# Kernel optimization log

Measured on AMD Instinct MI355X. Metric: run time of the kernel, lower is better.

Reference implementation:

```python
import jax, jax.numpy as jnp
import numpy as np
from jax import lax

N_KERNELS = 10000
KS = 9
DILATIONS = (1, 2, 4, 8, 16)   # static dilation groups, 2000 kernels each
GROUP = N_KERNELS // len(DILATIONS)
BN_EPS = 1e-5


def setup_inputs() -> dict:
    key = jax.random.key(0)
    kx, kw, kb, klw = jax.random.split(key, 4)
    B, L, C, n_class = 16, 256, 3, 10
    x_enc = jax.random.normal(kx, (B, L, C), dtype=jnp.float32)
    # ROCKET kernels: normal weights, mean-centered per kernel
    W = jax.random.normal(kw, (N_KERNELS, C, KS), dtype=jnp.float32)
    W = W - W.mean(axis=(1, 2), keepdims=True)
    # ROCKET biases: uniform(-1, 1)
    b = jax.random.uniform(kb, (N_KERNELS,), dtype=jnp.float32) * 2.0 - 1.0
    gamma = jnp.ones((2 * N_KERNELS,), dtype=jnp.float32)
    beta = jnp.zeros((2 * N_KERNELS,), dtype=jnp.float32)
    linW = jax.random.normal(klw, (2 * N_KERNELS, n_class), dtype=jnp.float32) * 0.01
    linB = jnp.zeros((n_class,), dtype=jnp.float32)
    return {"x_enc": x_enc, "W": W, "b": b, "gamma": gamma, "beta": beta,
            "linW": linW, "linB": linB}


def _rocket_features(x, W, b):
    # x: [B, C, L]; W: [N_KERNELS, C, KS]; b: [N_KERNELS]
    feats = []
    dn = ("NCH", "OIH", "NCH")
    for i, d in enumerate(DILATIONS):
        w = W[i * GROUP:(i + 1) * GROUP]                       # [G, C, KS]
        bb = b[i * GROUP:(i + 1) * GROUP]                      # [G]
        y = lax.conv_general_dilated(x, w, window_strides=(1,),
                                     padding="SAME", rhs_dilation=(d,),
                                     dimension_numbers=dn)      # [B, G, L]
        y = y + bb[None, :, None]
        feats.append(y.max(axis=-1))                            # max pooling
        feats.append(jnp.where(y > 0, 1.0, 0.0).mean(axis=-1))  # PPV
    return jnp.concatenate(feats, axis=-1)                      # [B, 2*N_KERNELS]


def reference(x_enc, W, b, gamma, beta, linW, linB):
    x = jnp.transpose(x_enc, (0, 2, 1))        # [B, C, L]
    feat = _rocket_features(x, W, b)           # [B, 20000]
    # BatchNorm1d (training mode: batch statistics, biased variance)
    mu = feat.mean(axis=0)
    var = feat.var(axis=0)
    feat_n = (feat - mu) * lax.rsqrt(var + BN_EPS) * gamma + beta
    return feat_n @ linW + linB                # [B, num_class]
```

## Files before the change

kernel.cpp:

```cpp
#include <hip/hip_runtime.h>
#include <cmath>

#define NK       10000
#define GROUP    2000
#define SEQ_L    256
#define FEAT_DIM 20000
#define NBATCH   16

typedef _Float16 half8 __attribute__((ext_vector_type(8)));
typedef float    f32x4 __attribute__((ext_vector_type(4)));

__launch_bounds__(128)
__global__ void rocket_mfma(const float* __restrict__ x_enc,
                            const float* __restrict__ Wk,
                            const float* __restrict__ bias,
                            float* __restrict__ feat)
{
    __shared__ __align__(16) float     xp[3 * 384];
    __shared__ __align__(16) _Float16  Bh[4 * 256 * 8];
    __shared__ __align__(16) _Float16  Bl[4 * 256 * 8];

    const int mt  = blockIdx.x;
    const int gi  = blockIdx.y;
    const int b   = blockIdx.z;
    const int d   = 1 << gi;
    const int tid = threadIdx.x;
    const int l   = tid & 63;
    const int wv  = tid >> 6;
    const int kb  = l >> 4;
    const int lr  = l & 15;

    for (int i = tid; i < 3 * 384; i += 128) xp[i] = 0.f;
    __syncthreads();
    for (int e = tid; e < SEQ_L * 3; e += 128) {
        const int t = e / 3;
        const int c = e - t * 3;
        xp[c * 384 + 64 + t] = x_enc[(b * SEQ_L + t) * 3 + c];
    }

    float awf[4][8];
#pragma unroll
    for (int tt = 0; tt < 4; ++tt) {
        const int nl = mt * 128 + wv * 64 + tt * 16 + lr;
        const int n  = gi * GROUP + (nl < GROUP ? nl : GROUP - 1);
#pragma unroll
        for (int j = 0; j < 8; ++j) {
            const int k = kb * 8 + j;
            awf[tt][j] = (k < 27) ? Wk[n * 27 + k] : 0.f;
        }
    }
    half8 ahi[4], alo[4];
#pragma unroll
    for (int tt = 0; tt < 4; ++tt)
#pragma unroll
        for (int j = 0; j < 8; ++j) {
            const _Float16 h = (_Float16)awf[tt][j];
            ahi[tt][j] = h;
            alo[tt][j] = (_Float16)(awf[tt][j] - (float)h);
        }
    float bsv[4][4];
#pragma unroll
    for (int tt = 0; tt < 4; ++tt)
#pragma unroll
        for (int r = 0; r < 4; ++r) {
            const int nl = mt * 128 + wv * 64 + tt * 16 + kb * 4 + r;
            bsv[tt][r] = bias[gi * GROUP + (nl < GROUP ? nl : GROUP - 1)];
        }

    __syncthreads();

    {
        const int kg = tid >> 5;
        const int tl = tid & 31;
#pragma unroll
        for (int i = 0; i < 8; ++i) {
            const int t = tl + 32 * i;
            half8 hv, lv;
#pragma unroll
            for (int kk = 0; kk < 8; ++kk) {
                const int k2 = kg * 8 + kk;
                float v = 0.f;
                if (k2 < 27) {
                    const int c  = (k2 >= 18) ? 2 : (k2 >= 9 ? 1 : 0);
                    const int k9 = k2 - c * 9;
                    v = xp[c * 384 + 64 + t + (k9 - 4) * d];
                }
                const _Float16 h = (_Float16)v;
                hv[kk] = h;
                lv[kk] = (_Float16)(v - (float)h);
            }
            *(half8*)&Bh[(kg * 256 + t) * 8] = hv;
            *(half8*)&Bl[(kg * 256 + t) * 8] = lv;
        }
    }
    __syncthreads();

    float mx[4][4], cnt[4][4];
#pragma unroll
    for (int tt = 0; tt < 4; ++tt)
#pragma unroll
        for (int r = 0; r < 4; ++r) { mx[tt][r] = -INFINITY; cnt[tt][r] = 0.f; }

#pragma unroll
    for (int ch = 0; ch < 16; ++ch) {
        const int t = ch * 16 + lr;
        const half8 bh = *(const half8*)&Bh[(kb * 256 + t) * 8];
        const half8 bl = *(const half8*)&Bl[(kb * 256 + t) * 8];
#pragma unroll
        for (int tt = 0; tt < 4; ++tt) {
            f32x4 acc = {0.f, 0.f, 0.f, 0.f};
            acc = __builtin_amdgcn_mfma_f32_16x16x32_f16(ahi[tt], bh, acc, 0, 0, 0);
            acc = __builtin_amdgcn_mfma_f32_16x16x32_f16(alo[tt], bh, acc, 0, 0, 0);
            acc = __builtin_amdgcn_mfma_f32_16x16x32_f16(ahi[tt], bl, acc, 0, 0, 0);
#pragma unroll
            for (int r = 0; r < 4; ++r) {
                const float y = acc[r] + bsv[tt][r];
                mx[tt][r]  = fmaxf(mx[tt][r], y);
                cnt[tt][r] += (y > 0.f) ? 1.f : 0.f;
            }
        }
    }

#pragma unroll
    for (int tt = 0; tt < 4; ++tt)
#pragma unroll
        for (int r = 0; r < 4; ++r) {
#pragma unroll
            for (int m = 1; m < 16; m <<= 1) {
                mx[tt][r]  = fmaxf(mx[tt][r], __shfl_xor(mx[tt][r], m));
                cnt[tt][r] += __shfl_xor(cnt[tt][r], m);
            }
        }

    if (lr == 0) {
        float* fb = feat + b * FEAT_DIM + gi * 4000;
#pragma unroll
        for (int tt = 0; tt < 4; ++tt)
#pragma unroll
            for (int r = 0; r < 4; ++r) {
                const int nl = mt * 128 + wv * 64 + tt * 16 + kb * 4 + r;
                if (nl < GROUP) {
                    fb[nl]         = mx[tt][r];
                    fb[2000 + nl]  = cnt[tt][r] * (1.0f / 256.0f);
                }
            }
    }
}

__launch_bounds__(256)
__global__ void bn_gemv(const float* __restrict__ feat,
                        const float* __restrict__ gamma,
                        const float* __restrict__ beta,
                        const float* __restrict__ linW,
                        float* __restrict__ partial)
{
    __shared__ float gs[625], hs[625];
    const int sl  = blockIdx.x;
    const int f0  = sl * 625;
    const int tid = threadIdx.x;

    for (int i = tid; i < 625; i += 256) {
        const int f = f0 + i;
        float s = 0.f, ss = 0.f;
#pragma unroll
        for (int b = 0; b < NBATCH; ++b) {
            const float v = feat[b * FEAT_DIM + f];
            s += v; ss += v * v;
        }
        const float mu  = s * (1.f / NBATCH);
        const float var = ss * (1.f / NBATCH) - mu * mu;
        const float gg  = gamma[f] * rsqrtf(var + 1e-5f);
        gs[i] = gg;
        hs[i] = beta[f] - mu * gg;
    }
    __syncthreads();

    const int bb = tid >> 4;
    const int ft = tid & 15;
    float acc[10];
#pragma unroll
    for (int c = 0; c < 10; ++c) acc[c] = 0.f;

    for (int i = ft; i < 625; i += 16) {
        const int f = f0 + i;
        const float tv = fmaf(feat[bb * FEAT_DIM + f], gs[i], hs[i]);
#pragma unroll
        for (int c = 0; c < 10; ++c) acc[c] = fmaf(tv, linW[f * 10 + c], acc[c]);
    }
#pragma unroll
    for (int c = 0; c < 10; ++c)
#pragma unroll
        for (int m = 1; m < 16; m <<= 1) acc[c] += __shfl_xor(acc[c], m);

    if (ft == 0) {
#pragma unroll
        for (int c = 0; c < 10; ++c)
            partial[(sl * NBATCH + bb) * 10 + c] = acc[c];
    }
}

__launch_bounds__(160)
__global__ void gemv_final(const float* __restrict__ partial,
                           const float* __restrict__ linB,
                           float* __restrict__ out)
{
    const int tid = threadIdx.x;
    const int c   = tid % 10;
    float s = linB[c];
#pragma unroll
    for (int sl = 0; sl < 32; ++sl) s += partial[sl * 160 + tid];
    out[tid] = s;
}

extern "C" void kernel_launch(void* const* d_in, const int* in_sizes, int n_in,
                              void* d_out, int out_size, void* d_ws, size_t ws_size,
                              hipStream_t stream) {
    const float* x     = (const float*)d_in[0];
    const float* Wk    = (const float*)d_in[1];
    const float* bias  = (const float*)d_in[2];
    const float* gamma = (const float*)d_in[3];
    const float* beta  = (const float*)d_in[4];
    const float* linW  = (const float*)d_in[5];
    const float* linB  = (const float*)d_in[6];
    float* out = (float*)d_out;

    float* feat    = (float*)d_ws;
    float* partial = feat + NBATCH * FEAT_DIM;

    rocket_mfma<<<dim3(16, 5, NBATCH), 128, 0, stream>>>(x, Wk, bias, feat);
    bn_gemv<<<dim3(32), 256, 0, stream>>>(feat, gamma, beta, linW, partial);
    gemv_final<<<dim3(1), 160, 0, stream>>>(partial, linB, out);
}
```

Baseline: 42.93 us.

## Precompute im2col fp16 split B tiles once per batch/dilation; widen BN-GEMV grid

Moves construction of the dilated im2col B operand (hi/lo fp16 split) out of the MFMA kernel into a separate build_B kernel. That kernel writes the operand once per (dilation, batch) to workspace, so the 16 M-tile blocks no longer each rebuild it in LDS and can read it straight from global/L2. The BN+GEMV stage is split into 80 slices of 250 features instead of 32 slices of 625, giving more parallelism. The cost is an extra kernel launch plus global memory traffic for the B operand.

Result: faster. 36.28 us (-15.5%).

```diff
diff --git a/kernel.cpp b/kernel.cpp
--- a/kernel.cpp
+++ b/kernel.cpp
@@ -10,35 +10,68 @@
 typedef _Float16 half8 __attribute__((ext_vector_type(8)));
 typedef float    f32x4 __attribute__((ext_vector_type(4)));
 
+__launch_bounds__(256)
+__global__ void build_B(const float* __restrict__ x_enc,
+                        _Float16* __restrict__ Bh_g,
+                        _Float16* __restrict__ Bl_g)
+{
+    __shared__ __align__(16) float xp[3 * 384];
+    const int gi  = blockIdx.x;
+    const int b   = blockIdx.y;
+    const int d   = 1 << gi;
+    const int tid = threadIdx.x;
+
+    for (int i = tid; i < 3 * 384; i += 256) xp[i] = 0.f;
+    __syncthreads();
+    for (int e = tid; e < SEQ_L * 3; e += 256) {
+        const int t = e / 3;
+        const int c = e - t * 3;
+        xp[c * 384 + 64 + t] = x_enc[(b * SEQ_L + t) * 3 + c];
+    }
+    __syncthreads();
+
+    const int base = (gi * NBATCH + b) * 1024;
+#pragma unroll
+    for (int q = 0; q < 4; ++q) {
+        const int idx = q * 256 + tid;
+        const int kb  = idx >> 8;
+        const int t   = idx & 255;
+        half8 hv, lv;
+#pragma unroll
+        for (int kk = 0; kk < 8; ++kk) {
+            const int k2 = kb * 8 + kk;
+            float v = 0.f;
+            if (k2 < 27) {
+                const int c  = (k2 >= 18) ? 2 : (k2 >= 9 ? 1 : 0);
+                const int k9 = k2 - c * 9;
+                v = xp[c * 384 + 64 + t + (k9 - 4) * d];
+            }
+            const _Float16 h = (_Float16)v;
+            hv[kk] = h;
+            lv[kk] = (_Float16)(v - (float)h);
+        }
+        *(half8*)&Bh_g[(base + idx) * 8] = hv;
+        *(half8*)&Bl_g[(base + idx) * 8] = lv;
+    }
+}
+
 __launch_bounds__(128)
-__global__ void rocket_mfma(const float* __restrict__ x_enc,
-                            const float* __restrict__ Wk,
-                            const float* __restrict__ bias,
-                            float* __restrict__ feat)
-{
-    __shared__ __align__(16) float     xp[3 * 384];
-    __shared__ __align__(16) _Float16  Bh[4 * 256 * 8];
-    __shared__ __align__(16) _Float16  Bl[4 * 256 * 8];
-
+__global__ void gemm_feat(const _Float16* __restrict__ Bh_g,
+                          const _Float16* __restrict__ Bl_g,
+                          const float* __restrict__ Wk,
+                          const float* __restrict__ bias,
+                          float* __restrict__ feat)
+{
     const int mt  = blockIdx.x;
     const int gi  = blockIdx.y;
     const int b   = blockIdx.z;
-    const int d   = 1 << gi;
     const int tid = threadIdx.x;
     const int l   = tid & 63;
     const int wv  = tid >> 6;
     const int kb  = l >> 4;
     const int lr  = l & 15;
 
-    for (int i = tid; i < 3 * 384; i += 128) xp[i] = 0.f;
-    __syncthreads();
-    for (int e = tid; e < SEQ_L * 3; e += 128) {
-        const int t = e / 3;
-        const int c = e - t * 3;
-        xp[c * 384 + 64 + t] = x_enc[(b * SEQ_L + t) * 3 + c];
-    }
-
-    float awf[4][8];
+    half8 ahi[4], alo[4];
 #pragma unroll
     for (int tt = 0; tt < 4; ++tt) {
         const int nl = mt * 128 + wv * 64 + tt * 16 + lr;
@@ -46,18 +79,12 @@
 #pragma unroll
         for (int j = 0; j < 8; ++j) {
             const int k = kb * 8 + j;
-            awf[tt][j] = (k < 27) ? Wk[n * 27 + k] : 0.f;
-        }
-    }
-    half8 ahi[4], alo[4];
-#pragma unroll
-    for (int tt = 0; tt < 4; ++tt)
-#pragma unroll
-        for (int j = 0; j < 8; ++j) {
-            const _Float16 h = (_Float16)awf[tt][j];
+            const float w = (k < 27) ? Wk[n * 27 + k] : 0.f;
+            const _Float16 h = (_Float16)w;
             ahi[tt][j] = h;
-            alo[tt][j] = (_Float16)(awf[tt][j] - (float)h);
-        }
+            alo[tt][j] = (_Float16)(w - (float)h);
+        }
+    }
     float bsv[4][4];
 #pragma unroll
     for (int tt = 0; tt < 4; ++tt)
@@ -67,33 +94,8 @@
             bsv[tt][r] = bias[gi * GROUP + (nl < GROUP ? nl : GROUP - 1)];
         }
 
-    __syncthreads();
-
-    {
-        const int kg = tid >> 5;
-        const int tl = tid & 31;
-#pragma unroll
-        for (int i = 0; i < 8; ++i) {
-            const int t = tl + 32 * i;
-            half8 hv, lv;
-#pragma unroll
-            for (int kk = 0; kk < 8; ++kk) {
-                const int k2 = kg * 8 + kk;
-                float v = 0.f;
-                if (k2 < 27) {
-                    const int c  = (k2 >= 18) ? 2 : (k2 >= 9 ? 1 : 0);
-                    const int k9 = k2 - c * 9;
-                    v = xp[c * 384 + 64 + t + (k9 - 4) * d];
-                }
-                const _Float16 h = (_Float16)v;
-                hv[kk] = h;
-                lv[kk] = (_Float16)(v - (float)h);
-            }
-            *(half8*)&Bh[(kg * 256 + t) * 8] = hv;
-            *(half8*)&Bl[(kg * 256 + t) * 8] = lv;
-        }
-    }
-    __syncthreads();
+    const _Float16* bhp = Bh_g + ((gi * NBATCH + b) * 1024 + kb * 256) * 8;
+    const _Float16* blp = Bl_g + ((gi * NBATCH + b) * 1024 + kb * 256) * 8;
 
     float mx[4][4], cnt[4][4];
 #pragma unroll
@@ -104,8 +106,8 @@
 #pragma unroll
     for (int ch = 0; ch < 16; ++ch) {
         const int t = ch * 16 + lr;
-        const half8 bh = *(const half8*)&Bh[(kb * 256 + t) * 8];
-        const half8 bl = *(const half8*)&Bl[(kb * 256 + t) * 8];
+        const half8 bh = *(const half8*)&bhp[t * 8];
+        const half8 bl = *(const half8*)&blp[t * 8];
 #pragma unroll
         for (int tt = 0; tt < 4; ++tt) {
             f32x4 acc = {0.f, 0.f, 0.f, 0.f};
@@ -140,8 +142,8 @@
             for (int r = 0; r < 4; ++r) {
                 const int nl = mt * 128 + wv * 64 + tt * 16 + kb * 4 + r;
                 if (nl < GROUP) {
-                    fb[nl]         = mx[tt][r];
-                    fb[2000 + nl]  = cnt[tt][r] * (1.0f / 256.0f);
+                    fb[nl]        = mx[tt][r];
+                    fb[2000 + nl] = cnt[tt][r] * (1.0f / 256.0f);
                 }
             }
     }
@@ -154,13 +156,13 @@
                         const float* __restrict__ linW,
                         float* __restrict__ partial)
 {
-    __shared__ float gs[625], hs[625];
+    __shared__ float gs[250], hs[250];
     const int sl  = blockIdx.x;
-    const int f0  = sl * 625;
-    const int tid = threadIdx.x;
-
-    for (int i = tid; i < 625; i += 256) {
-        const int f = f0 + i;
+    const int f0  = sl * 250;
+    const int tid = threadIdx.x;
+
+    if (tid < 250) {
+        const int f = f0 + tid;
         float s = 0.f, ss = 0.f;
 #pragma unroll
         for (int b = 0; b < NBATCH; ++b) {
@@ -170,8 +172,8 @@
         const float mu  = s * (1.f / NBATCH);
         const float var = ss * (1.f / NBATCH) - mu * mu;
         const float gg  = gamma[f] * rsqrtf(var + 1e-5f);
-        gs[i] = gg;
-        hs[i] = beta[f] - mu * gg;
+        gs[tid] = gg;
+        hs[tid] = beta[f] - mu * gg;
     }
     __syncthreads();
 
@@ -181,7 +183,7 @@
 #pragma unroll
     for (int c = 0; c < 10; ++c) acc[c] = 0.f;
 
-    for (int i = ft; i < 625; i += 16) {
+    for (int i = ft; i < 250; i += 16) {
         const int f = f0 + i;
         const float tv = fmaf(feat[bb * FEAT_DIM + f], gs[i], hs[i]);
 #pragma unroll
@@ -208,7 +210,7 @@
     const int c   = tid % 10;
     float s = linB[c];
 #pragma unroll
-    for (int sl = 0; sl < 32; ++sl) s += partial[sl * 160 + tid];
+    for (int sl = 0; sl < 80; ++sl) s += partial[sl * 160 + tid];
     out[tid] = s;
 }
 
@@ -224,10 +226,13 @@
     const float* linB  = (const float*)d_in[6];
     float* out = (float*)d_out;
 
-    float* feat    = (float*)d_ws;
-    float* partial = feat + NBATCH * FEAT_DIM;
-
-    rocket_mfma<<<dim3(16, 5, NBATCH), 128, 0, stream>>>(x, Wk, bias, feat);
-    bn_gemv<<<dim3(32), 256, 0, stream>>>(feat, gamma, beta, linW, partial);
+    float*    feat    = (float*)d_ws;
+    float*    partial = feat + NBATCH * FEAT_DIM;
+    _Float16* Bh      = (_Float16*)(partial + 80 * 160);
+    _Float16* Bl      = Bh + 5 * NBATCH * 1024 * 8;
+
+    build_B<<<dim3(5, NBATCH), 256, 0, stream>>>(x, Bh, Bl);
+    gemm_feat<<<dim3(16, 5, NBATCH), 128, 0, stream>>>(Bh, Bl, Wk, bias, feat);
+    bn_gemv<<<dim3(80), 256, 0, stream>>>(feat, gamma, beta, linW, partial);
     gemv_final<<<dim3(1), 160, 0, stream>>>(partial, linB, out);
 }
```
